# Kernel optimization log

Hardware: AMD Instinct MI355X
Metric: run time of the kernel (lower is better)

The kernel has to match this reference:

```python
import jax, jax.numpy as jnp
import numpy as np

B, I, H, O = 65536, 128, 256, 256

def setup_inputs() -> dict:
    key = jax.random.key(0)
    ks = jax.random.split(key, 6)
    s_h = 1.0 / np.sqrt(I + H)
    return {
        "input": jax.random.normal(ks[0], (B, I), jnp.float32),
        "hidden": jax.random.normal(ks[1], (B, H), jnp.float32),
        "w_i2h": jax.random.uniform(ks[2], (4 * H, I + H), jnp.float32, -s_h, s_h),
        "b_i2h": jax.random.uniform(ks[3], (4 * H,), jnp.float32, -s_h, s_h),
        "w_i2o": jax.random.uniform(ks[4], (O, I + H), jnp.float32, -s_h, s_h),
        "b_i2o": jax.random.uniform(ks[5], (O,), jnp.float32, -s_h, s_h),
    }

def reference(input, hidden, w_i2h, b_i2h, w_i2o, b_i2o):
    # combined: [B, I+H]
    combined = jnp.concatenate([input, hidden], axis=1)
    gates = combined @ w_i2h.T + b_i2h            # [B, 4H]
    h, ig, fg, og = jnp.split(gates, 4, axis=1)   # each [B, H]
    ig = jax.nn.sigmoid(ig)
    fg = jax.nn.sigmoid(fg)
    og = jax.nn.sigmoid(og)
    h = jnp.tanh(h)
    new_hidden = og * jnp.tanh(fg * hidden + ig * h)
    output = jax.nn.log_softmax(combined @ w_i2o.T + b_i2o, axis=1)  # [B, O]
    return (output, new_hidden)
```

## Files before the change

### kernel.cpp

```cpp
#include <hip/hip_runtime.h>
#include <hip/hip_bf16.h>
#include <math.h>


typedef __attribute__((ext_vector_type(8))) short bf16x8;
typedef __attribute__((ext_vector_type(4))) float f32x4;

#define BM   64
#define LDA  392
#define NW1  393216
#define NW2  98304

__device__ __forceinline__ unsigned short f2bf(float f) {
    union { __hip_bfloat16 h; unsigned short u; } cv;
    cv.h = __float2bfloat16(f);
    return cv.u;
}
__device__ __forceinline__ float bf2f(unsigned short u) {
    union { __hip_bfloat16 h; unsigned short u; } cv;
    cv.u = u;
    return __bfloat162float(cv.h);
}
__device__ __forceinline__ float fsigmoid(float x) {
    return 1.0f / (1.0f + __expf(-x));
}
__device__ __forceinline__ float ftanh(float x) {
    return 1.0f - 2.0f / (__expf(2.0f * x) + 1.0f);
}

__global__ void conv_w(const float* __restrict__ w1, const float* __restrict__ w2,
                       unsigned short* __restrict__ wb) {
    int idx = blockIdx.x * 256 + threadIdx.x;
    const int n1 = NW1 / 4;
    float4 v;
    if (idx < n1) v = ((const float4*)w1)[idx];
    else          v = ((const float4*)w2)[idx - n1];
    ushort4 u;
    u.x = f2bf(v.x); u.y = f2bf(v.y); u.z = f2bf(v.z); u.w = f2bf(v.w);
    ((ushort4*)wb)[idx] = u;
}

__launch_bounds__(256, 2)
__global__ void lstm_fused(const float* __restrict__ input,
                           const float* __restrict__ hidden,
                           const unsigned short* __restrict__ w1b,
                           const unsigned short* __restrict__ w2b,
                           const float* __restrict__ b1,
                           const float* __restrict__ b2,
                           float* __restrict__ out_ls,
                           float* __restrict__ out_nh)
{
    __shared__ unsigned short A[BM * LDA];
    __shared__ float red_m[4][BM];
    __shared__ float red_s[4][BM];

    const int tid  = threadIdx.x;
    const int wave = tid >> 6;
    const int lane = tid & 63;
    const int l15  = lane & 15;
    const int quad = lane >> 4;
    const size_t r0 = (size_t)blockIdx.x * BM;

    for (int idx = tid; idx < BM * 96; idx += 256) {
        int row = idx / 96, c4 = idx % 96;
        float4 v = (c4 < 32)
            ? ((const float4*)(input  + (r0 + row) * 128))[c4]
            : ((const float4*)(hidden + (r0 + row) * 256))[c4 - 32];
        ushort4 u;
        u.x = f2bf(v.x); u.y = f2bf(v.y); u.z = f2bf(v.z); u.w = f2bf(v.w);
        *(ushort4*)&A[row * LDA + c4 * 4] = u;
    }
    __syncthreads();

    const unsigned short* ap0 = &A[l15 * LDA + quad * 8];

    for (int phase = 0; phase < 5; ++phase) {
        f32x4 acc[4][4];
        #pragma unroll
        for (int i = 0; i < 4; ++i)
            #pragma unroll
            for (int j = 0; j < 4; ++j)
                acc[i][j] = (f32x4){0.f, 0.f, 0.f, 0.f};

        const unsigned short* bp[4];
        if (phase < 4) {
            int j0 = phase * 64 + wave * 16;
            #pragma unroll
            for (int q = 0; q < 4; ++q)
                bp[q] = w1b + (size_t)(q * 256 + j0 + l15) * 384 + quad * 8;
        } else {
            #pragma unroll
            for (int nt = 0; nt < 4; ++nt)
                bp[nt] = w2b + (size_t)(wave * 64 + nt * 16 + l15) * 384 + quad * 8;
        }

        #pragma unroll
        for (int kk = 0; kk < 384; kk += 32) {
            bf16x8 a[4], b[4];
            #pragma unroll
            for (int mt = 0; mt < 4; ++mt)
                a[mt] = *(const bf16x8*)(ap0 + mt * 16 * LDA + kk);
            #pragma unroll
            for (int nt = 0; nt < 4; ++nt)
                b[nt] = *(const bf16x8*)(bp[nt] + kk);
            #pragma unroll
            for (int mt = 0; mt < 4; ++mt)
                #pragma unroll
                for (int nt = 0; nt < 4; ++nt)
                    acc[mt][nt] = __builtin_amdgcn_mfma_f32_16x16x32_bf16(
                        a[mt], b[nt], acc[mt][nt], 0, 0, 0);
        }

        if (phase < 4) {
            int j = phase * 64 + wave * 16 + l15;
            float bq0 = b1[j], bq1 = b1[256 + j], bq2 = b1[512 + j], bq3 = b1[768 + j];
            #pragma unroll
            for (int mt = 0; mt < 4; ++mt) {
                #pragma unroll
                for (int r = 0; r < 4; ++r) {
                    int rowl = mt * 16 + quad * 4 + r;
                    float hprev = bf2f(A[rowl * LDA + 128 + j]);
                    float hv  = ftanh(acc[mt][0][r] + bq0);
                    float igv = fsigmoid(acc[mt][1][r] + bq1);
                    float fgv = fsigmoid(acc[mt][2][r] + bq2);
                    float ogv = fsigmoid(acc[mt][3][r] + bq3);
                    out_nh[(r0 + rowl) * 256 + j] = ogv * ftanh(fgv * hprev + igv * hv);
                }
            }
        } else {
            float bo[4];
            #pragma unroll
            for (int nt = 0; nt < 4; ++nt) bo[nt] = b2[wave * 64 + nt * 16 + l15];
            #pragma unroll
            for (int mt = 0; mt < 4; ++mt)
                #pragma unroll
                for (int nt = 0; nt < 4; ++nt)
                    #pragma unroll
                    for (int r = 0; r < 4; ++r)
                        acc[mt][nt][r] += bo[nt];

            float pm[4][4], ps[4][4];
            #pragma unroll
            for (int mt = 0; mt < 4; ++mt)
                #pragma unroll
                for (int r = 0; r < 4; ++r) {
                    float m = acc[mt][0][r];
                    #pragma unroll
                    for (int nt = 1; nt < 4; ++nt) m = fmaxf(m, acc[mt][nt][r]);
                    pm[mt][r] = m;
                }
            #pragma unroll
            for (int mask = 1; mask < 16; mask <<= 1)
                #pragma unroll
                for (int mt = 0; mt < 4; ++mt)
                    #pragma unroll
                    for (int r = 0; r < 4; ++r)
                        pm[mt][r] = fmaxf(pm[mt][r], __shfl_xor(pm[mt][r], mask, 64));
            #pragma unroll
            for (int mt = 0; mt < 4; ++mt)
                #pragma unroll
                for (int r = 0; r < 4; ++r) {
                    float s = 0.f;
                    #pragma unroll
                    for (int nt = 0; nt < 4; ++nt)
                        s += __expf(acc[mt][nt][r] - pm[mt][r]);
                    ps[mt][r] = s;
                }
            #pragma unroll
            for (int mask = 1; mask < 16; mask <<= 1)
                #pragma unroll
                for (int mt = 0; mt < 4; ++mt)
                    #pragma unroll
                    for (int r = 0; r < 4; ++r)
                        ps[mt][r] += __shfl_xor(ps[mt][r], mask, 64);

            if (l15 == 0) {
                #pragma unroll
                for (int mt = 0; mt < 4; ++mt)
                    #pragma unroll
                    for (int r = 0; r < 4; ++r) {
                        int rowl = mt * 16 + quad * 4 + r;
                        red_m[wave][rowl] = pm[mt][r];
                        red_s[wave][rowl] = ps[mt][r];
                    }
            }
            __syncthreads();
            #pragma unroll
            for (int mt = 0; mt < 4; ++mt)
                #pragma unroll
                for (int r = 0; r < 4; ++r) {
                    int rowl = mt * 16 + quad * 4 + r;
                    float M = red_m[0][rowl];
                    #pragma unroll
                    for (int w = 1; w < 4; ++w) M = fmaxf(M, red_m[w][rowl]);
                    float S = 0.f;
                    #pragma unroll
                    for (int w = 0; w < 4; ++w)
                        S += red_s[w][rowl] * __expf(red_m[w][rowl] - M);
                    float lz = M + logf(S);
                    #pragma unroll
                    for (int nt = 0; nt < 4; ++nt)
                        out_ls[(r0 + rowl) * 256 + wave * 64 + nt * 16 + l15] =
                            acc[mt][nt][r] - lz;
                }
        }
    }
}

extern "C" void kernel_launch(void* const* d_in, const int* in_sizes, int n_in,
                              void* d_out, int out_size, void* d_ws, size_t ws_size,
                              hipStream_t stream) {
    const float* input  = (const float*)d_in[0];
    const float* hidden = (const float*)d_in[1];
    const float* w1     = (const float*)d_in[2];
    const float* b1     = (const float*)d_in[3];
    const float* w2     = (const float*)d_in[4];
    const float* b2     = (const float*)d_in[5];
    float* out = (float*)d_out;
    unsigned short* wb = (unsigned short*)d_ws;

    conv_w<<<dim3((NW1 + NW2) / 4 / 256), dim3(256), 0, stream>>>(w1, w2, wb);
    lstm_fused<<<dim3(65536 / BM), dim3(256), 0, stream>>>(
        input, hidden, wb, wb + NW1, b1, b2,
        out, out + (size_t)65536 * 256);
}
```

Baseline: 331.4 us.

## Swizzle LDS layout, double-buffer weight loads, raise occupancy to three blocks

Replaces the padded LDS row stride with an unpadded 768-byte row and an XOR swizzle of 16-byte groups, cutting shared memory per block and avoiding bank conflicts on the A-fragment reads. The staging loop now loads 8 floats per thread and writes packed bf16x8 vectors. The K loop is restructured to prefetch the next B (weight) fragments from global memory while the current MFMAs run, and launch bounds ask for 3 blocks per CU. The risks are extra register pressure from the double-buffered fragments under the tighter occupancy bound, and possible spills.

After: 377.5 us. +13.9%, slower.

```diff
diff --git a/kernel.cpp b/kernel.cpp
--- a/kernel.cpp
+++ b/kernel.cpp
@@ -7,7 +7,6 @@
 typedef __attribute__((ext_vector_type(4))) float f32x4;
 
 #define BM   64
-#define LDA  392
 #define NW1  393216
 #define NW2  98304
 
@@ -26,6 +25,14 @@
 }
 __device__ __forceinline__ float ftanh(float x) {
     return 1.0f - 2.0f / (__expf(2.0f * x) + 1.0f);
+}
+__device__ __forceinline__ bf16x8 pack8(float4 v0, float4 v1) {
+    bf16x8 r;
+    r[0] = (short)f2bf(v0.x); r[1] = (short)f2bf(v0.y);
+    r[2] = (short)f2bf(v0.z); r[3] = (short)f2bf(v0.w);
+    r[4] = (short)f2bf(v1.x); r[5] = (short)f2bf(v1.y);
+    r[6] = (short)f2bf(v1.z); r[7] = (short)f2bf(v1.w);
+    return r;
 }
 
 __global__ void conv_w(const float* __restrict__ w1, const float* __restrict__ w2,
@@ -40,7 +47,11 @@
     ((ushort4*)wb)[idx] = u;
 }
 
-__launch_bounds__(256, 2)
+__device__ __forceinline__ int lds_off(int row, int g) {
+    return row * 768 + ((g ^ (row & 7)) << 4);
+}
+
+__launch_bounds__(256, 3)
 __global__ void lstm_fused(const float* __restrict__ input,
                            const float* __restrict__ hidden,
                            const unsigned short* __restrict__ w1b,
@@ -50,29 +61,32 @@
                            float* __restrict__ out_ls,
                            float* __restrict__ out_nh)
 {
-    __shared__ unsigned short A[BM * LDA];
+    __shared__ __align__(16) unsigned short Ash[BM * 384];
     __shared__ float red_m[4][BM];
     __shared__ float red_s[4][BM];
+    char* Ab = (char*)Ash;
 
     const int tid  = threadIdx.x;
     const int wave = tid >> 6;
     const int lane = tid & 63;
     const int l15  = lane & 15;
     const int quad = lane >> 4;
+    const int rx   = l15 & 7;
     const size_t r0 = (size_t)blockIdx.x * BM;
 
-    for (int idx = tid; idx < BM * 96; idx += 256) {
-        int row = idx / 96, c4 = idx % 96;
-        float4 v = (c4 < 32)
-            ? ((const float4*)(input  + (r0 + row) * 128))[c4]
-            : ((const float4*)(hidden + (r0 + row) * 256))[c4 - 32];
-        ushort4 u;
-        u.x = f2bf(v.x); u.y = f2bf(v.y); u.z = f2bf(v.z); u.w = f2bf(v.w);
-        *(ushort4*)&A[row * LDA + c4 * 4] = u;
+    #pragma unroll
+    for (int it = 0; it < 12; ++it) {
+        int idx = it * 256 + tid;
+        int row = idx / 48, g = idx % 48;
+        const float* src = (g < 16) ? (input  + (r0 + row) * 128 + g * 8)
+                                    : (hidden + (r0 + row) * 256 + (g - 16) * 8);
+        float4 v0 = ((const float4*)src)[0];
+        float4 v1 = ((const float4*)src)[1];
+        *(bf16x8*)(Ab + lds_off(row, g)) = pack8(v0, v1);
     }
     __syncthreads();
 
-    const unsigned short* ap0 = &A[l15 * LDA + quad * 8];
+    const int abase = l15 * 768;
 
     for (int phase = 0; phase < 5; ++phase) {
         f32x4 acc[4][4];
@@ -94,32 +108,49 @@
                 bp[nt] = w2b + (size_t)(wave * 64 + nt * 16 + l15) * 384 + quad * 8;
         }
 
-        #pragma unroll
-        for (int kk = 0; kk < 384; kk += 32) {
-            bf16x8 a[4], b[4];
-            #pragma unroll
-            for (int mt = 0; mt < 4; ++mt)
-                a[mt] = *(const bf16x8*)(ap0 + mt * 16 * LDA + kk);
+        auto loadB = [&](bf16x8* b, int kk) {
             #pragma unroll
             for (int nt = 0; nt < 4; ++nt)
                 b[nt] = *(const bf16x8*)(bp[nt] + kk);
+        };
+        auto loadA = [&](bf16x8* a, int kk) {
+            int go = (((kk >> 3) + quad) ^ rx) << 4;
+            #pragma unroll
+            for (int mt = 0; mt < 4; ++mt)
+                a[mt] = *(const bf16x8*)(Ab + abase + mt * 12288 + go);
+        };
+        auto mfmas = [&](bf16x8* a, bf16x8* b) {
             #pragma unroll
             for (int mt = 0; mt < 4; ++mt)
                 #pragma unroll
                 for (int nt = 0; nt < 4; ++nt)
                     acc[mt][nt] = __builtin_amdgcn_mfma_f32_16x16x32_bf16(
                         a[mt], b[nt], acc[mt][nt], 0, 0, 0);
+        };
+
+        bf16x8 b0[4], b1f[4], a0[4], a1[4];
+        loadB(b0, 0);
+        #pragma unroll
+        for (int kk = 0; kk < 384; kk += 64) {
+            loadB(b1f, kk + 32);
+            loadA(a0, kk);
+            mfmas(a0, b0);
+            if (kk + 64 < 384) loadB(b0, kk + 64);
+            loadA(a1, kk + 32);
+            mfmas(a1, b1f);
         }
 
         if (phase < 4) {
             int j = phase * 64 + wave * 16 + l15;
             float bq0 = b1[j], bq1 = b1[256 + j], bq2 = b1[512 + j], bq3 = b1[768 + j];
+            int e = 128 + j, ge = e >> 3, oe = (e & 7) * 2;
             #pragma unroll
             for (int mt = 0; mt < 4; ++mt) {
                 #pragma unroll
                 for (int r = 0; r < 4; ++r) {
                     int rowl = mt * 16 + quad * 4 + r;
-                    float hprev = bf2f(A[rowl * LDA + 128 + j]);
+                    float hprev = bf2f(*(const unsigned short*)
+                                       (Ab + lds_off(rowl, ge) + oe));
                     float hv  = ftanh(acc[mt][0][r] + bq0);
                     float igv = fsigmoid(acc[mt][1][r] + bq1);
                     float fgv = fsigmoid(acc[mt][2][r] + bq2);
```
